# Kernel tuning notes

Hardware: AMD Instinct MI355X
Metric: run time of the kernel (lower is better)

## Reference

```python
import jax, jax.numpy as jnp
import numpy as np

N_NODES = 100000
N_EDGES = 1600000
D_IN = 128
HIDDEN = 128
N_LAYERS = 4


def setup_inputs() -> dict:
    key = jax.random.key(0)
    ks = jax.random.split(key, 32)

    def lin(k, fan_in, fan_out):
        return (jax.random.normal(k, (fan_in, fan_out), jnp.float32) / np.float32(np.sqrt(fan_in)))

    inp = {}
    inp["x"] = jax.random.normal(ks[0], (N_NODES, D_IN), jnp.float32)
    inp["edge_index"] = jax.random.randint(ks[1], (2, N_EDGES), 0, N_NODES, dtype=jnp.int32)
    # pre_mp: Linear(input_dim, hidden_dim)
    inp["pre_w"] = lin(ks[2], D_IN, HIDDEN)
    inp["pre_b"] = jnp.zeros((HIDDEN,), jnp.float32)
    # convs: GCNConv(hidden*(l+1), hidden), skip='all'
    for l in range(N_LAYERS):
        inp[f"conv_w{l}"] = lin(ks[3 + l], HIDDEN * (l + 1), HIDDEN)
        inp[f"conv_b{l}"] = jnp.zeros((HIDDEN,), jnp.float32)
    # post_mp: Linear(hidden*(L+1), hidden) -> LeakyReLU(0.1) -> Linear(hidden, hidden) -> ReLU -> Linear(hidden, 256) -> ReLU -> Linear(256, hidden)
    inp["post_w1"] = lin(ks[10], HIDDEN * (N_LAYERS + 1), HIDDEN)
    inp["post_b1"] = jnp.zeros((HIDDEN,), jnp.float32)
    inp["post_w2"] = lin(ks[11], HIDDEN, HIDDEN)
    inp["post_b2"] = jnp.zeros((HIDDEN,), jnp.float32)
    inp["post_w3"] = lin(ks[12], HIDDEN, 256)
    inp["post_b3"] = jnp.zeros((256,), jnp.float32)
    inp["post_w4"] = lin(ks[13], 256, HIDDEN)
    inp["post_b4"] = jnp.zeros((HIDDEN,), jnp.float32)
    return inp


def reference(x, edge_index, pre_w, pre_b,
              conv_w0, conv_b0, conv_w1, conv_b1,
              conv_w2, conv_b2, conv_w3, conv_b3,
              post_w1, post_b1, post_w2, post_b2,
              post_w3, post_b3, post_w4, post_b4):
    n = x.shape[0]
    src, dst = edge_index[0], edge_index[1]
    loop = jnp.arange(n, dtype=src.dtype)
    # GCNConv default: add self-loops, symmetric normalization (same every layer)
    src2 = jnp.concatenate([src, loop])
    dst2 = jnp.concatenate([dst, loop])
    deg = jax.ops.segment_sum(jnp.ones(src2.shape[0], x.dtype), dst2, num_segments=n)
    dinv = jnp.where(deg > 0, jax.lax.rsqrt(deg), 0.0)
    norm = dinv[src2] * dinv[dst2]  # [E + N]

    def gcn(h, W, b):
        h = h @ W                                   # linear transform first (as in PyG GCNConv)
        msg = norm[:, None] * h[src2]               # gather + normalize
        agg = jax.ops.segment_sum(msg, dst2, num_segments=n)  # scatter-add
        return agg + b

    emb = x @ pre_w + pre_b  # pre_mp
    for W, b in ((conv_w0, conv_b0), (conv_w1, conv_b1), (conv_w2, conv_b2), (conv_w3, conv_b3)):
        h = jax.nn.relu(gcn(emb, W, b))  # skip='all': conv consumes full concat; dropout is identity in eval
        emb = jnp.concatenate([emb, h], axis=1)

    # post_mp (Dropout identity in eval)
    h = emb @ post_w1 + post_b1
    h = jnp.where(h > 0, h, 0.1 * h)  # LeakyReLU(0.1)
    h = jax.nn.relu(h @ post_w2 + post_b2)
    h = jax.nn.relu(h @ post_w3 + post_b3)
    return h @ post_w4 + post_b4
```

## Files before the change

kernel.cpp:

```cpp
#include <hip/hip_runtime.h>


typedef __bf16 bf16;
typedef __attribute__((ext_vector_type(8))) __bf16 bf16x8;
typedef __attribute__((ext_vector_type(4))) float f32x4;

__global__ __launch_bounds__(256) void zero_int(int* p, int n) {
    int i = blockIdx.x * 256 + threadIdx.x;
    if (i < n) p[i] = 0;
}

__global__ __launch_bounds__(256) void hist_dst(const int* __restrict__ ei,
                                                int* cnt, int* __restrict__ rank, int E) {
    int e = blockIdx.x * 256 + threadIdx.x;
    if (e < E) rank[e] = atomicAdd(&cnt[ei[E + e]], 1);
}

__global__ __launch_bounds__(256) void scan1(const int* __restrict__ cnt,
                                             int* __restrict__ rp,
                                             float* __restrict__ dinv,
                                             int* __restrict__ bsum, int n) {
    __shared__ int sums[256];
    const int t = threadIdx.x;
    const int base = blockIdx.x * 1024 + t * 4;
    int4 v = make_int4(0, 0, 0, 0);
    if (base < n) v = *(const int4*)&cnt[base];
    int s = v.x + v.y + v.z + v.w;
    sums[t] = s;
    __syncthreads();
#pragma unroll
    for (int off = 1; off < 256; off <<= 1) {
        int u = (t >= off) ? sums[t - off] : 0;
        __syncthreads();
        sums[t] += u;
        __syncthreads();
    }
    int excl = sums[t] - s;
    if (base < n) {
        int4 r;
        r.x = excl;
        r.y = r.x + v.x;
        r.z = r.y + v.y;
        r.w = r.z + v.z;
        *(int4*)&rp[base] = r;
        float4 dv;
        dv.x = rsqrtf((float)(v.x + 1));
        dv.y = rsqrtf((float)(v.y + 1));
        dv.z = rsqrtf((float)(v.z + 1));
        dv.w = rsqrtf((float)(v.w + 1));
        *(float4*)&dinv[base] = dv;
    }
    if (t == 255) bsum[blockIdx.x] = sums[255];
}

__global__ __launch_bounds__(128) void scan2(int* __restrict__ bsum, int nb) {
    __shared__ int sums[128];
    const int t = threadIdx.x;
    int s = (t < nb) ? bsum[t] : 0;
    sums[t] = s;
    __syncthreads();
#pragma unroll
    for (int off = 1; off < 128; off <<= 1) {
        int u = (t >= off) ? sums[t - off] : 0;
        __syncthreads();
        sums[t] += u;
        __syncthreads();
    }
    if (t < nb) bsum[t] = sums[t] - s;
}

__global__ __launch_bounds__(256) void scan3(int* __restrict__ rp,
                                             const int* __restrict__ bsum, int n, int E) {
    const int base = blockIdx.x * 1024 + threadIdx.x * 4;
    if (base < n) {
        int o = bsum[blockIdx.x];
        int4 r = *(int4*)&rp[base];
        r.x += o; r.y += o; r.z += o; r.w += o;
        *(int4*)&rp[base] = r;
    }
    if (blockIdx.x == 0 && threadIdx.x == 0) rp[n] = E;
}

__global__ __launch_bounds__(256) void csr_fill(const int* __restrict__ ei,
                                                const int* __restrict__ rp,
                                                const int* __restrict__ rank,
                                                int* __restrict__ csr, int E) {
    const int T = gridDim.x * 256;
    int e = blockIdx.x * 256 + threadIdx.x;
#pragma unroll 4
    for (int i = 0; i < 4; ++i) {
        if (e < E) csr[rp[ei[E + e]] + rank[e]] = ei[e];
        e += T;
    }
}

struct TAll {
    const float* src[9];
    int cum[10];
    int N[9];
    int K[9];
};
__global__ __launch_bounds__(256) void transpose_all(TAll d, bf16* __restrict__ wt, int total) {
    int idx = blockIdx.x * 256 + threadIdx.x;
    if (idx >= total) return;
    int seg = 0;
#pragma unroll
    for (int s = 1; s < 9; ++s) if (idx >= d.cum[s]) seg = s;
    int local = idx - d.cum[seg];
    int N = d.N[seg], K = d.K[seg];
    int k = local / N;
    int nn = local - k * N;
    wt[d.cum[seg] + (size_t)nn * K + k] = (bf16)d.src[seg][local];
}

__device__ __forceinline__ void stash_lds(char* H, int ktStride, int r, int c, float v) {
    int kt = c >> 6, w = c & 63;
    int byte = kt * ktStride + r * 128 + (((w >> 3) ^ (r & 7)) * 8 + (w & 7)) * 2;
    *(bf16*)(H + byte) = (bf16)v;
}
__device__ __forceinline__ bf16x8 afrag_lds(const char* H, int ktStride, int kt, int r, int ks, int lane) {
    int ch = (ks * 4 + (lane >> 4)) ^ (r & 7);
    return *(const bf16x8*)(H + kt * ktStride + r * 128 + ch * 16);
}

__global__ __launch_bounds__(256) void gemm_bf16(
    const bf16* __restrict__ A1, int lda1, int K1,
    const bf16* __restrict__ A2, int lda2,
    const bf16* __restrict__ WT,
    const float* __restrict__ bias,
    const float* __restrict__ rowscale,
    void* __restrict__ Cout, int ldc, int M, int Ktot,
    int act, int outf32)
{
    __shared__ bf16 Als[128 * 64];
    __shared__ bf16 Bls[128 * 64];

    const int t = threadIdx.x;
    const int lane = t & 63;
    const int wid = t >> 6;
    const int wm = wid >> 1, wn = wid & 1;
    const int row0 = blockIdx.x * 128;
    const int col0 = blockIdx.y * 128;
    const int nt = Ktot >> 6;

    f32x4 acc[4][4];
#pragma unroll
    for (int mf = 0; mf < 4; ++mf)
#pragma unroll
        for (int nf = 0; nf < 4; ++nf) {
            f32x4 z = {0.f, 0.f, 0.f, 0.f};
            acc[mf][nf] = z;
        }

    int srow[4], scs[4];
#pragma unroll
    for (int i = 0; i < 4; ++i) {
        int ch = wid * 64 + i * 256 + lane;
        int row = ch >> 3, c = ch & 7;
        srow[i] = row;
        scs[i] = (c ^ (row & 7)) * 8;
    }

    for (int kt = 0; kt < nt; ++kt) {
        const int k0 = kt * 64;
        const bf16* Ap; int lda_, kk;
        if (k0 < K1) { Ap = A1; lda_ = lda1; kk = k0; }
        else         { Ap = A2; lda_ = lda2; kk = k0 - K1; }

        __syncthreads();
#pragma unroll
        for (int i = 0; i < 4; ++i) {
            int grow = row0 + srow[i]; if (grow >= M) grow = M - 1;
            const bf16* ga = &Ap[(size_t)grow * lda_ + kk + scs[i]];
            const bf16* gb = &WT[(size_t)(col0 + srow[i]) * Ktot + k0 + scs[i]];
            bf16* la = &Als[(size_t)(wid * 64 + i * 256) * 8];
            bf16* lb = &Bls[(size_t)(wid * 64 + i * 256) * 8];
            __builtin_amdgcn_global_load_lds(
                (const __attribute__((address_space(1))) void*)ga,
                (__attribute__((address_space(3))) void*)la, 16, 0, 0);
            __builtin_amdgcn_global_load_lds(
                (const __attribute__((address_space(1))) void*)gb,
                (__attribute__((address_space(3))) void*)lb, 16, 0, 0);
        }
        asm volatile("s_waitcnt vmcnt(0)" ::: "memory");
        __syncthreads();

#pragma unroll
        for (int ks = 0; ks < 2; ++ks) {
            bf16x8 af[4], bfr[4];
#pragma unroll
            for (int mf = 0; mf < 4; ++mf) {
                int r = wm * 64 + mf * 16 + (lane & 15);
                int ch = (ks * 4 + (lane >> 4)) ^ (r & 7);
                af[mf] = *(const bf16x8*)((const char*)Als + r * 128 + ch * 16);
            }
#pragma unroll
            for (int nf = 0; nf < 4; ++nf) {
                int r = wn * 64 + nf * 16 + (lane & 15);
                int ch = (ks * 4 + (lane >> 4)) ^ (r & 7);
                bfr[nf] = *(const bf16x8*)((const char*)Bls + r * 128 + ch * 16);
            }
#pragma unroll
            for (int mf = 0; mf < 4; ++mf)
#pragma unroll
                for (int nf = 0; nf < 4; ++nf)
                    acc[mf][nf] = __builtin_amdgcn_mfma_f32_16x16x32_bf16(
                        af[mf], bfr[nf], acc[mf][nf], 0, 0, 0);
        }
    }

#pragma unroll
    for (int mf = 0; mf < 4; ++mf) {
        int rbase = row0 + wm * 64 + mf * 16 + (lane >> 4) * 4;
#pragma unroll
        for (int nf = 0; nf < 4; ++nf) {
            int gcol = col0 + wn * 64 + nf * 16 + (lane & 15);
            float bv = bias ? bias[gcol] : 0.f;
#pragma unroll
            for (int i = 0; i < 4; ++i) {
                int grow = rbase + i;
                if (grow >= M) continue;
                float v = acc[mf][nf][i];
                if (rowscale) v *= rowscale[grow];
                v += bv;
                if (act == 1) v = fmaxf(v, 0.f);
                else if (act == 2) v = v > 0.f ? v : 0.1f * v;
                if (outf32) ((float*)Cout)[(size_t)grow * ldc + gcol] = v;
                else        ((bf16*)Cout)[(size_t)grow * ldc + gcol] = (bf16)v;
            }
        }
    }
}

__global__ __launch_bounds__(256) void fused_pre(
    const float* __restrict__ x,
    const bf16* __restrict__ preWT,
    const float* __restrict__ pre_b,
    const bf16* __restrict__ c0WT,
    const float* __restrict__ dinv,
    bf16* __restrict__ emb, int lde,
    bf16* __restrict__ g, int M)
{
    __shared__ char lds[49152];
    bf16* Hbuf = (bf16*)lds;
    bf16* Bls  = (bf16*)(lds + 32768);
    bf16* Als  = Hbuf;

    const int t = threadIdx.x;
    const int lane = t & 63;
    const int wid = t >> 6;
    const int wm = wid >> 1, wn = wid & 1;
    const int row0 = blockIdx.x * 128;

    int srow[4], scs[4];
#pragma unroll
    for (int i = 0; i < 4; ++i) {
        int ch = wid * 64 + i * 256 + lane;
        int row = ch >> 3, c = ch & 7;
        srow[i] = row;
        scs[i] = (c ^ (row & 7)) * 8;
    }

    f32x4 acc[4][4];
#pragma unroll
    for (int mf = 0; mf < 4; ++mf)
#pragma unroll
        for (int nf = 0; nf < 4; ++nf) { f32x4 z = {0,0,0,0}; acc[mf][nf] = z; }

    for (int kt = 0; kt < 2; ++kt) {
        __syncthreads();
#pragma unroll
        for (int i = 0; i < 4; ++i) {
            int grow = row0 + srow[i]; if (grow >= M) grow = M - 1;
            const float* gx = &x[(size_t)grow * 128 + kt * 64 + scs[i]];
            float4 f0 = *(const float4*)gx;
            float4 f1 = *(const float4*)(gx + 4);
            bf16x8 av = {(bf16)f0.x, (bf16)f0.y, (bf16)f0.z, (bf16)f0.w,
                         (bf16)f1.x, (bf16)f1.y, (bf16)f1.z, (bf16)f1.w};
            *(bf16x8*)((char*)Als + (size_t)(wid * 64 + i * 256 + lane) * 16) = av;
            const bf16* gb = &preWT[(size_t)srow[i] * 128 + kt * 64 + scs[i]];
            bf16* lb = &Bls[(size_t)(wid * 64 + i * 256) * 8];
            __builtin_amdgcn_global_load_lds(
                (const __attribute__((address_space(1))) void*)gb,
                (__attribute__((address_space(3))) void*)lb, 16, 0, 0);
        }
        asm volatile("s_waitcnt vmcnt(0)" ::: "memory");
        __syncthreads();
#pragma unroll
        for (int ks = 0; ks < 2; ++ks) {
            bf16x8 af[4], bfr[4];
#pragma unroll
            for (int mf = 0; mf < 4; ++mf) {
                int r = wm * 64 + mf * 16 + (lane & 15);
                int ch = (ks * 4 + (lane >> 4)) ^ (r & 7);
                af[mf] = *(const bf16x8*)((const char*)Als + r * 128 + ch * 16);
            }
#pragma unroll
            for (int nf = 0; nf < 4; ++nf) {
                int r = wn * 64 + nf * 16 + (lane & 15);
                int ch = (ks * 4 + (lane >> 4)) ^ (r & 7);
                bfr[nf] = *(const bf16x8*)((const char*)Bls + r * 128 + ch * 16);
            }
#pragma unroll
            for (int mf = 0; mf < 4; ++mf)
#pragma unroll
                for (int nf = 0; nf < 4; ++nf)
                    acc[mf][nf] = __builtin_amdgcn_mfma_f32_16x16x32_bf16(
                        af[mf], bfr[nf], acc[mf][nf], 0, 0, 0);
        }
    }
    __syncthreads();

#pragma unroll
    for (int mf = 0; mf < 4; ++mf) {
        int rl = wm * 64 + mf * 16 + (lane >> 4) * 4;
#pragma unroll
        for (int nf = 0; nf < 4; ++nf) {
            int c = wn * 64 + nf * 16 + (lane & 15);
            float bv = pre_b[c];
#pragma unroll
            for (int i = 0; i < 4; ++i) {
                int r = rl + i;
                float v = acc[mf][nf][i] + bv;
                stash_lds((char*)Hbuf, 16384, r, c, v);
                int grow = row0 + r;
                if (grow < M) emb[(size_t)grow * lde + c] = (bf16)v;
            }
        }
    }

#pragma unroll
    for (int mf = 0; mf < 4; ++mf)
#pragma unroll
        for (int nf = 0; nf < 4; ++nf) { f32x4 z = {0,0,0,0}; acc[mf][nf] = z; }

    for (int kt = 0; kt < 2; ++kt) {
        __syncthreads();
#pragma unroll
        for (int i = 0; i < 4; ++i) {
            const bf16* gb = &c0WT[(size_t)srow[i] * 128 + kt * 64 + scs[i]];
            bf16* lb = &Bls[(size_t)(wid * 64 + i * 256) * 8];
            __builtin_amdgcn_global_load_lds(
                (const __attribute__((address_space(1))) void*)gb,
                (__attribute__((address_space(3))) void*)lb, 16, 0, 0);
        }
        asm volatile("s_waitcnt vmcnt(0)" ::: "memory");
        __syncthreads();
#pragma unroll
        for (int ks = 0; ks < 2; ++ks) {
            bf16x8 af[4], bfr[4];
#pragma unroll
            for (int mf = 0; mf < 4; ++mf) {
                int r = wm * 64 + mf * 16 + (lane & 15);
                af[mf] = afrag_lds((const char*)Hbuf, 16384, kt, r, ks, lane);
            }
#pragma unroll
            for (int nf = 0; nf < 4; ++nf) {
                int r = wn * 64 + nf * 16 + (lane & 15);
                int ch = (ks * 4 + (lane >> 4)) ^ (r & 7);
                bfr[nf] = *(const bf16x8*)((const char*)Bls + r * 128 + ch * 16);
            }
#pragma unroll
            for (int mf = 0; mf < 4; ++mf)
#pragma unroll
                for (int nf = 0; nf < 4; ++nf)
                    acc[mf][nf] = __builtin_amdgcn_mfma_f32_16x16x32_bf16(
                        af[mf], bfr[nf], acc[mf][nf], 0, 0, 0);
        }
    }

#pragma unroll
    for (int mf = 0; mf < 4; ++mf) {
        int rbase = row0 + wm * 64 + mf * 16 + (lane >> 4) * 4;
#pragma unroll
        for (int nf = 0; nf < 4; ++nf) {
            int c = wn * 64 + nf * 16 + (lane & 15);
#pragma unroll
            for (int i = 0; i < 4; ++i) {
                int grow = rbase + i;
                if (grow >= M) continue;
                g[(size_t)grow * 128 + c] = (bf16)(acc[mf][nf][i] * dinv[grow]);
            }
        }
    }
}

__global__ __launch_bounds__(256) void fused_post(
    const bf16* __restrict__ h1,
    const bf16* __restrict__ W2T,
    const float* __restrict__ b2,
    const bf16* __restrict__ W3T,
    const float* __restrict__ b3,
    const bf16* __restrict__ W4T,
    const float* __restrict__ b4,
    float* __restrict__ out, int M)
{
    __shared__ char lds[49152];
    bf16* H2  = (bf16*)lds;
    bf16* Bls = (bf16*)(lds + 16384);
    bf16* H3  = (bf16*)(lds + 32768);
    bf16* Als = H3;

    const int t = threadIdx.x;
    const int lane = t & 63;
    const int wid = t >> 6;
    const int wm = wid >> 1, wn = wid & 1;
    const int row0 = blockIdx.x * 64;

    int srow[4], scs[4];
#pragma unroll
    for (int i = 0; i < 4; ++i) {
        int ch = wid * 64 + i * 256 + lane;
        int row = ch >> 3, c = ch & 7;
        srow[i] = row;
        scs[i] = (c ^ (row & 7)) * 8;
    }

    f32x4 acc[2][4], acc3[2][4];
#pragma unroll
    for (int mf = 0; mf < 2; ++mf)
#pragma unroll
        for (int nf = 0; nf < 4; ++nf) {
            f32x4 z = {0,0,0,0};
            acc[mf][nf] = z;
            acc3[mf][nf] = z;
        }

    for (int kt = 0; kt < 2; ++kt) {
        __syncthreads();
#pragma unroll
        for (int i = 0; i < 2; ++i) {
            int grow = row0 + srow[i]; if (grow >= M) grow = M - 1;
            const bf16* ga = &h1[(size_t)grow * 128 + kt * 64 + scs[i]];
            bf16* la = &Als[(size_t)(wid * 64 + i * 256) * 8];
            __builtin_amdgcn_global_load_lds(
                (const __attribute__((address_space(1))) void*)ga,
                (__attribute__((address_space(3))) void*)la, 16, 0, 0);
        }
#pragma unroll
        for (int i = 0; i < 4; ++i) {
            const bf16* gb = &W2T[(size_t)srow[i] * 128 + kt * 64 + scs[i]];
            bf16* lb = &Bls[(size_t)(wid * 64 + i * 256) * 8];
            __builtin_amdgcn_global_load_lds(
                (const __attribute__((address_space(1))) void*)gb,
                (__attribute__((address_space(3))) void*)lb, 16, 0, 0);
        }
        asm volatile("s_waitcnt vmcnt(0)" ::: "memory");
        __syncthreads();
#pragma unroll
        for (int ks = 0; ks < 2; ++ks) {
            bf16x8 af[2], bfr[4];
#pragma unroll
            for (int mf = 0; mf < 2; ++mf) {
                int r = wm * 32 + mf * 16 + (lane & 15);
                int ch = (ks * 4 + (lane >> 4)) ^ (r & 7);
                af[mf] = *(const bf16x8*)((const char*)Als + r * 128 + ch * 16);
            }
#pragma unroll
            for (int nf = 0; nf < 4; ++nf) {
                int r = wn * 64 + nf * 16 + (lane & 15);
                int ch = (ks * 4 + (lane >> 4)) ^ (r & 7);
                bfr[nf] = *(const bf16x8*)((const char*)Bls + r * 128 + ch * 16);
            }
#pragma unroll
            for (int mf = 0; mf < 2; ++mf)
#pragma unroll
                for (int nf = 0; nf < 4; ++nf)
                    acc[mf][nf] = __builtin_amdgcn_mfma_f32_16x16x32_bf16(
                        af[mf], bfr[nf], acc[mf][nf], 0, 0, 0);
        }
    }
    __syncthreads();
#pragma unroll
    for (int mf = 0; mf < 2; ++mf) {
        int rl = wm * 32 + mf * 16 + (lane >> 4) * 4;
#pragma unroll
        for (int nf = 0; nf < 4; ++nf) {
            int c = wn * 64 + nf * 16 + (lane & 15);
            float bv = b2[c];
#pragma unroll
            for (int i = 0; i < 4; ++i)
                stash_lds((char*)H2, 8192, rl + i, c, fmaxf(acc[mf][nf][i] + bv, 0.f));
        }
    }

    for (int hh = 0; hh < 2; ++hh) {
#pragma unroll
        for (int mf = 0; mf < 2; ++mf)
#pragma unroll
            for (int nf = 0; nf < 4; ++nf) { f32x4 z = {0,0,0,0}; acc[mf][nf] = z; }
        for (int kt = 0; kt < 2; ++kt) {
            __syncthreads();
#pragma unroll
            for (int i = 0; i < 4; ++i) {
                const bf16* gb = &W3T[(size_t)(hh * 128 + srow[i]) * 128 + kt * 64 + scs[i]];
                bf16* lb = &Bls[(size_t)(wid * 64 + i * 256) * 8];
                __builtin_amdgcn_global_load_lds(
                    (const __attribute__((address_space(1))) void*)gb,
                    (__attribute__((address_space(3))) void*)lb, 16, 0, 0);
            }
            asm volatile("s_waitcnt vmcnt(0)" ::: "memory");
            __syncthreads();
#pragma unroll
            for (int ks = 0; ks < 2; ++ks) {
                bf16x8 af[2], bfr[4];
#pragma unroll
                for (int mf = 0; mf < 2; ++mf) {
                    int r = wm * 32 + mf * 16 + (lane & 15);
                    af[mf] = afrag_lds((const char*)H2, 8192, kt, r, ks, lane);
                }
#pragma unroll
                for (int nf = 0; nf < 4; ++nf) {
                    int r = wn * 64 + nf * 16 + (lane & 15);
                    int ch = (ks * 4 + (lane >> 4)) ^ (r & 7);
                    bfr[nf] = *(const bf16x8*)((const char*)Bls + r * 128 + ch * 16);
                }
#pragma unroll
                for (int mf = 0; mf < 2; ++mf)
#pragma unroll
                    for (int nf = 0; nf < 4; ++nf)
                        acc[mf][nf] = __builtin_amdgcn_mfma_f32_16x16x32_bf16(
                            af[mf], bfr[nf], acc[mf][nf], 0, 0, 0);
            }
        }
        __syncthreads();
#pragma unroll
        for (int mf = 0; mf < 2; ++mf) {
            int rl = wm * 32 + mf * 16 + (lane >> 4) * 4;
#pragma unroll
            for (int nf = 0; nf < 4; ++nf) {
                int c = wn * 64 + nf * 16 + (lane & 15);
                float bv = b3[hh * 128 + c];
#pragma unroll
                for (int i = 0; i < 4; ++i)
                    stash_lds((char*)H3, 8192, rl + i, c, fmaxf(acc[mf][nf][i] + bv, 0.f));
            }
        }
        for (int kt = 0; kt < 2; ++kt) {
            __syncthreads();
#pragma unroll
            for (int i = 0; i < 4; ++i) {
                const bf16* gb = &W4T[(size_t)srow[i] * 256 + hh * 128 + kt * 64 + scs[i]];
                bf16* lb = &Bls[(size_t)(wid * 64 + i * 256) * 8];
                __builtin_amdgcn_global_load_lds(
                    (const __attribute__((address_space(1))) void*)gb,
                    (__attribute__((address_space(3))) void*)lb, 16, 0, 0);
            }
            asm volatile("s_waitcnt vmcnt(0)" ::: "memory");
            __syncthreads();
#pragma unroll
            for (int ks = 0; ks < 2; ++ks) {
                bf16x8 af[2], bfr[4];
#pragma unroll
                for (int mf = 0; mf < 2; ++mf) {
                    int r = wm * 32 + mf * 16 + (lane & 15);
                    af[mf] = afrag_lds((const char*)H3, 8192, kt, r, ks, lane);
                }
#pragma unroll
                for (int nf = 0; nf < 4; ++nf) {
                    int r = wn * 64 + nf * 16 + (lane & 15);
                    int ch = (ks * 4 + (lane >> 4)) ^ (r & 7);
                    bfr[nf] = *(const bf16x8*)((const char*)Bls + r * 128 + ch * 16);
                }
#pragma unroll
                for (int mf = 0; mf < 2; ++mf)
#pragma unroll
                    for (int nf = 0; nf < 4; ++nf)
                        acc3[mf][nf] = __builtin_amdgcn_mfma_f32_16x16x32_bf16(
                            af[mf], bfr[nf], acc3[mf][nf], 0, 0, 0);
            }
        }
    }

#pragma unroll
    for (int mf = 0; mf < 2; ++mf) {
        int rbase = row0 + wm * 32 + mf * 16 + (lane >> 4) * 4;
#pragma unroll
        for (int nf = 0; nf < 4; ++nf) {
            int c = wn * 64 + nf * 16 + (lane & 15);
            float bv = b4[c];
#pragma unroll
            for (int i = 0; i < 4; ++i) {
                int grow = rbase + i;
                if (grow < M) out[(size_t)grow * 128 + c] = acc3[mf][nf][i] + bv;
            }
        }
    }
}

__global__ __launch_bounds__(256) void gcn_gather(
    const int* __restrict__ rp, const int* __restrict__ csr,
    const bf16* __restrict__ g, const float* __restrict__ dinv,
    const float* __restrict__ b,
    bf16* __restrict__ out, int ldo, int n)
{
    const int node = (int)(((long long)blockIdx.x * 256 + threadIdx.x) >> 6);
    if (node >= n) return;
    const int lane = threadIdx.x & 63;
    const int grp = lane >> 4;
    const int cc = lane & 15;
    const int start = rp[node];
    const int end = rp[node + 1];

    float acc[8];
#pragma unroll
    for (int j = 0; j < 8; ++j) acc[j] = 0.f;

    int j = start + grp;
    for (; j + 12 < end; j += 16) {
        int s0 = csr[j];
        int s1 = csr[j + 4];
        int s2 = csr[j + 8];
        int s3 = csr[j + 12];
        bf16x8 v0 = *(const bf16x8*)&g[(size_t)s0 * 128 + cc * 8];
        bf16x8 v1 = *(const bf16x8*)&g[(size_t)s1 * 128 + cc * 8];
        bf16x8 v2 = *(const bf16x8*)&g[(size_t)s2 * 128 + cc * 8];
        bf16x8 v3 = *(const bf16x8*)&g[(size_t)s3 * 128 + cc * 8];
#pragma unroll
        for (int jj = 0; jj < 8; ++jj)
            acc[jj] += ((float)v0[jj] + (float)v1[jj]) + ((float)v2[jj] + (float)v3[jj]);
    }
    for (; j < end; j += 4) {
        int s0 = csr[j];
        bf16x8 v0 = *(const bf16x8*)&g[(size_t)s0 * 128 + cc * 8];
#pragma unroll
        for (int jj = 0; jj < 8; ++jj) acc[jj] += (float)v0[jj];
    }
#pragma unroll
    for (int jj = 0; jj < 8; ++jj) {
        acc[jj] += __shfl_xor(acc[jj], 16, 64);
        acc[jj] += __shfl_xor(acc[jj], 32, 64);
    }
    if (grp == 0) {
        bf16x8 sv = *(const bf16x8*)&g[(size_t)node * 128 + cc * 8];
        float s = dinv[node];
        bf16x8 o;
#pragma unroll
        for (int jj = 0; jj < 8; ++jj) {
            float v = fmaf(s, acc[jj] + (float)sv[jj], b[cc * 8 + jj]);
            o[jj] = (bf16)fmaxf(v, 0.f);
        }
        *(bf16x8*)&out[(size_t)node * ldo + cc * 8] = o;
    }
}

extern "C" void kernel_launch(void* const* d_in, const int* in_sizes, int n_in,
                              void* d_out, int out_size, void* d_ws, size_t ws_size,
                              hipStream_t stream) {
    const float* x      = (const float*)d_in[0];
    const int*   ei     = (const int*)d_in[1];
    const float* pre_w  = (const float*)d_in[2];
    const float* pre_b  = (const float*)d_in[3];
    const float* conv_w[4] = {(const float*)d_in[4], (const float*)d_in[6],
                              (const float*)d_in[8], (const float*)d_in[10]};
    const float* conv_b[4] = {(const float*)d_in[5], (const float*)d_in[7],
                              (const float*)d_in[9], (const float*)d_in[11]};
    const float* post_w1 = (const float*)d_in[12];
    const float* post_b1 = (const float*)d_in[13];
    const float* post_w2 = (const float*)d_in[14];
    const float* post_b2 = (const float*)d_in[15];
    const float* post_w3 = (const float*)d_in[16];
    const float* post_b3 = (const float*)d_in[17];
    const float* post_w4 = (const float*)d_in[18];
    const float* post_b4 = (const float*)d_in[19];

    const int n = in_sizes[0] / 128;
    const int E = in_sizes[1] / 2;
    const int nb = (n + 1023) / 1024;

    size_t off = 0;
    bf16* emb  = (bf16*)((char*)d_ws + off); off += (size_t)n * 512 * 2;
    bf16* g    = (bf16*)((char*)d_ws + off); off += (size_t)n * 128 * 2;
    bf16* h4   = (bf16*)((char*)d_ws + off); off += (size_t)n * 128 * 2;
    float* dinv = (float*)((char*)d_ws + off); off += (size_t)n * 4;
    int*   rp   = (int*)((char*)d_ws + off); off += (size_t)(n + 4) * 4;
    int*   csr  = (int*)((char*)d_ws + off); off += (size_t)E * 4;
    int*   rank = (int*)((char*)d_ws + off); off += (size_t)E * 4;
    bf16*  wt   = (bf16*)((char*)d_ws + off); off += (size_t)344064 * 2;
    int*   bsum = (int*)((char*)d_ws + off); off += 128 * 4;
    if (ws_size < off) return;

    int* cnt = (int*)dinv;
    bf16* h1 = g;

    bf16* pre_wt  = wt;
    bf16* c_wt0   = wt + 16384;
    bf16* c_wt1   = wt + 32768;
    bf16* c_wt2   = wt + 65536;
    bf16* c_wt3   = wt + 114688;
    bf16* p1_wt   = wt + 180224;
    bf16* p2_wt   = wt + 262144;
    bf16* p3_wt   = wt + 278528;
    bf16* p4_wt   = wt + 311296;
    bf16* c_wt[4] = {c_wt0, c_wt1, c_wt2, c_wt3};

    zero_int<<<(n + 255) / 256, 256, 0, stream>>>(cnt, n);
    hist_dst<<<(E + 255) / 256, 256, 0, stream>>>(ei, cnt, rank, E);
    scan1<<<nb, 256, 0, stream>>>(cnt, rp, dinv, bsum, n);
    scan2<<<1, 128, 0, stream>>>(bsum, nb);
    scan3<<<nb, 256, 0, stream>>>(rp, bsum, n, E);
    csr_fill<<<(E / 4 + 255) / 256, 256, 0, stream>>>(ei, rp, rank, csr, E);

    TAll ta;
    ta.src[0] = pre_w;   ta.K[0] = 128; ta.N[0] = 128;
    ta.src[1] = conv_w[0]; ta.K[1] = 128; ta.N[1] = 128;
    ta.src[2] = conv_w[1]; ta.K[2] = 256; ta.N[2] = 128;
    ta.src[3] = conv_w[2]; ta.K[3] = 384; ta.N[3] = 128;
    ta.src[4] = conv_w[3]; ta.K[4] = 512; ta.N[4] = 128;
    ta.src[5] = post_w1;  ta.K[5] = 640; ta.N[5] = 128;
    ta.src[6] = post_w2;  ta.K[6] = 128; ta.N[6] = 128;
    ta.src[7] = post_w3;  ta.K[7] = 128; ta.N[7] = 256;
    ta.src[8] = post_w4;  ta.K[8] = 256; ta.N[8] = 128;
    ta.cum[0] = 0;
    for (int s = 0; s < 9; ++s) ta.cum[s + 1] = ta.cum[s] + ta.K[s] * ta.N[s];
    const int wtot = ta.cum[9];
    transpose_all<<<(wtot + 255) / 256, 256, 0, stream>>>(ta, wt, wtot);

    const int gx = (n + 127) / 128;
    const int gx2 = (n + 63) / 64;
    auto gemm = [&](const bf16* A1, int lda1, int K1, const bf16* A2, int lda2,
                    const bf16* WT, const float* bias, const float* rs,
                    void* C, int ldc, int Ktot, int N, int act, int outf32) {
        dim3 grid(gx, N / 128);
        gemm_bf16<<<grid, 256, 0, stream>>>(A1, lda1, K1, A2, lda2, WT, bias, rs,
                                            C, ldc, n, Ktot, act, outf32);
    };

    const int ggrid = (int)(((long long)n * 64 + 255) / 256);
    for (int l = 0; l < 4; ++l) {
        if (l == 0) {
            fused_pre<<<gx, 256, 0, stream>>>(x, pre_wt, pre_b, c_wt0, dinv,
                                              emb, 512, g, n);
        } else {
            int K = 128 * (l + 1);
            gemm(emb, 512, K, emb, 512, c_wt[l], nullptr, dinv, g, 128, K, 128, 0, 0);
        }
        bf16* out = (l < 3) ? (emb + (size_t)128 * (l + 1)) : h4;
        int ldo = (l < 3) ? 512 : 128;
        gcn_gather<<<ggrid, 256, 0, stream>>>(rp, csr, g, dinv, conv_b[l], out, ldo, n);
    }

    gemm(emb, 512, 512, h4, 128, p1_wt, post_b1, nullptr, h1, 128, 640, 128, 2, 0);
    fused_post<<<gx2, 256, 0, stream>>>(h1, p2_wt, post_b2, p3_wt, post_b3,
                                        p4_wt, post_b4, (float*)d_out, n);
}
```

Baseline: 676.9 us.

## Build CSR via two-level bucketed partition instead of global atomic histogram

Replaces the global-atomic histogram, three-kernel scan and random CSR fill with a two-pass radix-style partition. Edges are first bucketed by dst>>9 using shared-memory counters and scattered as (src,dst) pairs, then each 512-node bucket builds its local CSR in shared memory. This is meant to avoid contended global atomics and scattered global writes. In exchange it adds an extra 8-byte-per-edge buffer and a second read pass over the edges. The order of neighbours within a row becomes nondeterministic, which can change floating-point summation order.

```diff
diff --git a/kernel.cpp b/kernel.cpp
--- a/kernel.cpp
+++ b/kernel.cpp
@@ -5,27 +5,54 @@
 typedef __attribute__((ext_vector_type(8))) __bf16 bf16x8;
 typedef __attribute__((ext_vector_type(4))) float f32x4;
 
-__global__ __launch_bounds__(256) void zero_int(int* p, int n) {
-    int i = blockIdx.x * 256 + threadIdx.x;
-    if (i < n) p[i] = 0;
-}
-
-__global__ __launch_bounds__(256) void hist_dst(const int* __restrict__ ei,
-                                                int* cnt, int* __restrict__ rank, int E) {
-    int e = blockIdx.x * 256 + threadIdx.x;
-    if (e < E) rank[e] = atomicAdd(&cnt[ei[E + e]], 1);
-}
-
-__global__ __launch_bounds__(256) void scan1(const int* __restrict__ cnt,
-                                             int* __restrict__ rp,
-                                             float* __restrict__ dinv,
-                                             int* __restrict__ bsum, int n) {
+#define BSHIFT 9
+#define PCHUNK 4096
+
+__global__ __launch_bounds__(256) void part_count(const int* __restrict__ ei,
+                                                  int* __restrict__ bcountT,
+                                                  int NBKT, int NBLK, int E) {
+    __shared__ int cnt[256];
+    const int t = threadIdx.x, blk = blockIdx.x;
+    if (t < NBKT) cnt[t] = 0;
+    __syncthreads();
+    const int base = blk * PCHUNK;
+#pragma unroll
+    for (int i = 0; i < 16; ++i) {
+        int e = base + i * 256 + t;
+        if (e < E) atomicAdd(&cnt[ei[E + e] >> BSHIFT], 1);
+    }
+    __syncthreads();
+    if (t < NBKT) bcountT[t * NBLK + blk] = cnt[t];
+}
+
+__global__ __launch_bounds__(256) void part_scanb(int* __restrict__ bcountT,
+                                                  int* __restrict__ btot, int NBLK) {
+    __shared__ int sums[256];
+    const int b = blockIdx.x, t = threadIdx.x;
+    int* row = &bcountT[(size_t)b * NBLK];
+    const int chunk = (NBLK + 255) / 256;
+    const int lo = t * chunk, hi = min(lo + chunk, NBLK);
+    int s = 0;
+    for (int i = lo; i < hi; ++i) s += row[i];
+    sums[t] = s;
+    __syncthreads();
+#pragma unroll
+    for (int off = 1; off < 256; off <<= 1) {
+        int u = (t >= off) ? sums[t - off] : 0;
+        __syncthreads();
+        sums[t] += u;
+        __syncthreads();
+    }
+    int run = sums[t] - s;
+    for (int i = lo; i < hi; ++i) { int c = row[i]; row[i] = run; run += c; }
+    if (t == 255) btot[b] = sums[255];
+}
+
+__global__ __launch_bounds__(256) void part_scant(const int* __restrict__ btot,
+                                                  int* __restrict__ bbase, int NBKT, int E) {
     __shared__ int sums[256];
     const int t = threadIdx.x;
-    const int base = blockIdx.x * 1024 + t * 4;
-    int4 v = make_int4(0, 0, 0, 0);
-    if (base < n) v = *(const int4*)&cnt[base];
-    int s = v.x + v.y + v.z + v.w;
+    int s = (t < NBKT) ? btot[t] : 0;
     sums[t] = s;
     __syncthreads();
 #pragma unroll
@@ -35,62 +62,71 @@
         sums[t] += u;
         __syncthreads();
     }
-    int excl = sums[t] - s;
-    if (base < n) {
-        int4 r;
-        r.x = excl;
-        r.y = r.x + v.x;
-        r.z = r.y + v.y;
-        r.w = r.z + v.z;
-        *(int4*)&rp[base] = r;
-        float4 dv;
-        dv.x = rsqrtf((float)(v.x + 1));
-        dv.y = rsqrtf((float)(v.y + 1));
-        dv.z = rsqrtf((float)(v.z + 1));
-        dv.w = rsqrtf((float)(v.w + 1));
-        *(float4*)&dinv[base] = dv;
-    }
-    if (t == 255) bsum[blockIdx.x] = sums[255];
-}
-
-__global__ __launch_bounds__(128) void scan2(int* __restrict__ bsum, int nb) {
-    __shared__ int sums[128];
-    const int t = threadIdx.x;
-    int s = (t < nb) ? bsum[t] : 0;
-    sums[t] = s;
-    __syncthreads();
-#pragma unroll
-    for (int off = 1; off < 128; off <<= 1) {
-        int u = (t >= off) ? sums[t - off] : 0;
-        __syncthreads();
-        sums[t] += u;
-        __syncthreads();
-    }
-    if (t < nb) bsum[t] = sums[t] - s;
-}
-
-__global__ __launch_bounds__(256) void scan3(int* __restrict__ rp,
-                                             const int* __restrict__ bsum, int n, int E) {
-    const int base = blockIdx.x * 1024 + threadIdx.x * 4;
-    if (base < n) {
-        int o = bsum[blockIdx.x];
-        int4 r = *(int4*)&rp[base];
-        r.x += o; r.y += o; r.z += o; r.w += o;
-        *(int4*)&rp[base] = r;
-    }
-    if (blockIdx.x == 0 && threadIdx.x == 0) rp[n] = E;
-}
-
-__global__ __launch_bounds__(256) void csr_fill(const int* __restrict__ ei,
-                                                const int* __restrict__ rp,
-                                                const int* __restrict__ rank,
-                                                int* __restrict__ csr, int E) {
-    const int T = gridDim.x * 256;
-    int e = blockIdx.x * 256 + threadIdx.x;
-#pragma unroll 4
-    for (int i = 0; i < 4; ++i) {
-        if (e < E) csr[rp[ei[E + e]] + rank[e]] = ei[e];
-        e += T;
+    if (t < NBKT) bbase[t] = sums[t] - s;
+    if (t == 0) bbase[NBKT] = E;
+}
+
+__global__ __launch_bounds__(256) void part_scatter(const int* __restrict__ ei,
+                                                    const int* __restrict__ bcountT,
+                                                    const int* __restrict__ bbase,
+                                                    int2* __restrict__ sorted,
+                                                    int NBKT, int NBLK, int E) {
+    __shared__ int cur[256];
+    const int t = threadIdx.x, blk = blockIdx.x;
+    if (t < NBKT) cur[t] = bbase[t] + bcountT[(size_t)t * NBLK + blk];
+    __syncthreads();
+    const int base = blk * PCHUNK;
+#pragma unroll
+    for (int i = 0; i < 16; ++i) {
+        int e = base + i * 256 + t;
+        if (e < E) {
+            int src = ei[e], dst = ei[E + e];
+            int pos = atomicAdd(&cur[dst >> BSHIFT], 1);
+            sorted[pos] = make_int2(src, dst);
+        }
+    }
+}
+
+__global__ __launch_bounds__(512) void bucket_csr(const int2* __restrict__ sorted,
+                                                  const int* __restrict__ bbase,
+                                                  int* __restrict__ rp,
+                                                  float* __restrict__ dinv,
+                                                  int* __restrict__ csr,
+                                                  int n, int E) {
+    __shared__ int cnt[512];
+    __shared__ int cur[512];
+    const int b = blockIdx.x, t = threadIdx.x;
+    const int nb0 = b << BSHIFT;
+    const int lo = bbase[b], hi = bbase[b + 1];
+    cnt[t] = 0;
+    __syncthreads();
+    for (int k = lo + t; k < hi; k += 512)
+        atomicAdd(&cnt[sorted[k].y - nb0], 1);
+    __syncthreads();
+    const int own = cnt[t];
+    cur[t] = own;
+    __syncthreads();
+#pragma unroll
+    for (int off = 1; off < 512; off <<= 1) {
+        int u = (t >= off) ? cur[t - off] : 0;
+        __syncthreads();
+        cur[t] += u;
+        __syncthreads();
+    }
+    const int excl = cur[t] - own;
+    const int node = nb0 + t;
+    if (node < n) {
+        rp[node] = lo + excl;
+        dinv[node] = rsqrtf((float)(own + 1));
+    }
+    if (b == 0 && t == 0) rp[n] = E;
+    __syncthreads();
+    cur[t] = excl;
+    __syncthreads();
+    for (int k = lo + t; k < hi; k += 512) {
+        int2 e = sorted[k];
+        int pos = atomicAdd(&cur[e.y - nb0], 1);
+        csr[lo + pos] = e.x;
     }
 }
 
@@ -666,7 +702,8 @@
 
     const int n = in_sizes[0] / 128;
     const int E = in_sizes[1] / 2;
-    const int nb = (n + 1023) / 1024;
+    const int NBKT = (n + 511) >> BSHIFT;
+    const int NBLK = (E + PCHUNK - 1) / PCHUNK;
 
     size_t off = 0;
     bf16* emb  = (bf16*)((char*)d_ws + off); off += (size_t)n * 512 * 2;
@@ -675,12 +712,13 @@
     float* dinv = (float*)((char*)d_ws + off); off += (size_t)n * 4;
     int*   rp   = (int*)((char*)d_ws + off); off += (size_t)(n + 4) * 4;
     int*   csr  = (int*)((char*)d_ws + off); off += (size_t)E * 4;
-    int*   rank = (int*)((char*)d_ws + off); off += (size_t)E * 4;
+    int2*  sorted = (int2*)((char*)d_ws + off); off += (size_t)E * 8;
     bf16*  wt   = (bf16*)((char*)d_ws + off); off += (size_t)344064 * 2;
-    int*   bsum = (int*)((char*)d_ws + off); off += 128 * 4;
+    int*   bcountT = (int*)((char*)d_ws + off); off += (size_t)NBKT * NBLK * 4;
+    int*   btot    = (int*)((char*)d_ws + off); off += (size_t)NBKT * 4;
+    int*   bbase   = (int*)((char*)d_ws + off); off += (size_t)(NBKT + 1) * 4;
     if (ws_size < off) return;
 
-    int* cnt = (int*)dinv;
     bf16* h1 = g;
 
     bf16* pre_wt  = wt;
@@ -694,12 +732,11 @@
     bf16* p4_wt   = wt + 311296;
     bf16* c_wt[4] = {c_wt0, c_wt1, c_wt2, c_wt3};
 
-    zero_int<<<(n + 255) / 256, 256, 0, stream>>>(cnt, n);
-    hist_dst<<<(E + 255) / 256, 256, 0, stream>>>(ei, cnt, rank, E);
-    scan1<<<nb, 256, 0, stream>>>(cnt, rp, dinv, bsum, n);
-    scan2<<<1, 128, 0, stream>>>(bsum, nb);
-    scan3<<<nb, 256, 0, stream>>>(rp, bsum, n, E);
-    csr_fill<<<(E / 4 + 255) / 256, 256, 0, stream>>>(ei, rp, rank, csr, E);
+    part_count<<<NBLK, 256, 0, stream>>>(ei, bcountT, NBKT, NBLK, E);
+    part_scanb<<<NBKT, 256, 0, stream>>>(bcountT, btot, NBLK);
+    part_scant<<<1, 256, 0, stream>>>(btot, bbase, NBKT, E);
+    part_scatter<<<NBLK, 256, 0, stream>>>(ei, bcountT, bbase, sorted, NBKT, NBLK, E);
+    bucket_csr<<<NBKT, 512, 0, stream>>>(sorted, bbase, rp, dinv, csr, n, E);
 
     TAll ta;
     ta.src[0] = pre_w;   ta.K[0] = 128; ta.N[0] = 128;
```

Measured after the change: 607.7 us. 10.2% less time.
